# Kernel tuning notes

Measured on AMD Instinct MI355X. Metric: run time of the kernel, lower is better.

## Reference

```python
import jax, jax.numpy as jnp
import numpy as np

M, B, U, D = 65536, 128, 256, 512
USAGE_DECAY = 0.95

def _l2n(x, axis):
    # tf.nn.l2_normalize semantics (K.l2_normalize)
    return x / jnp.sqrt(jnp.maximum(jnp.sum(x * x, axis=axis, keepdims=True), 1e-12))

def _lstm_cell(x, h, c, kernel, rec_kernel, bias):
    # Keras LSTMCell: gates in order i, f, c, o
    z = x @ kernel + h @ rec_kernel + bias  # [B, 4U]
    zi, zf, zc, zo = jnp.split(z, 4, axis=-1)
    i = jax.nn.sigmoid(zi)
    f = jax.nn.sigmoid(zf)
    c_new = f * c + i * jnp.tanh(zc)
    o = jax.nn.sigmoid(zo)
    h_new = o * jnp.tanh(c_new)
    return h_new, c_new

def setup_inputs() -> dict:
    key = jax.random.key(0)
    ks = jax.random.split(key, 10)
    return {
        "inputs": jax.random.normal(ks[0], (B, D), jnp.float32),
        "r_tm1": jnp.zeros((B, U), jnp.float32),
        "m_tm1": jax.random.uniform(ks[1], (M, U), jnp.float32),
        "c_wu_tm1": jax.random.uniform(ks[2], (M, B), jnp.float32),
        "c_wlu_tm1": jnp.zeros((M, B), jnp.float32),
        "c_wr_tm1": jax.random.uniform(ks[3], (M, B), jnp.float32),
        "h_tm1": jax.random.normal(ks[4], (B, U), jnp.float32) * 0.1,
        "cc_tm1": jax.random.normal(ks[5], (B, U), jnp.float32) * 0.1,
        "kernel": jax.random.normal(ks[6], (D + U, 4 * U), jnp.float32) * 0.02,
        "rec_kernel": jax.random.normal(ks[7], (U, 4 * U), jnp.float32) * 0.02,
        "bias": jnp.zeros((4 * U,), jnp.float32),
        "write_gate": jax.random.normal(ks[8], (1,), jnp.float32),
    }

def reference(inputs, r_tm1, m_tm1, c_wu_tm1, c_wlu_tm1, c_wr_tm1,
              h_tm1, cc_tm1, kernel, rec_kernel, bias, write_gate):
    # Controller step on [inputs, r_tm1]
    ctrl_in = jnp.concatenate([inputs, r_tm1], axis=1)          # [B, D+U]
    key_list, cc = _lstm_cell(ctrl_in, h_tm1, cc_tm1, kernel, rec_kernel, bias)  # [B, U]

    wg = jax.nn.sigmoid(write_gate)                              # [1]
    # NOTE: faithful to source -- scalar (1 - wg) is ADDED elementwise, then c_wlu added
    c_ww = wg * c_wr_tm1 + (1.0 - wg) + c_wlu_tm1                # [M, B]

    # cosine-similarity addressing
    cos = _l2n(key_list, 1) @ _l2n(m_tm1, 1).T                   # [B, M]
    # K.softmax on the transposed matrix => softmax over the BATCH axis (faithful)
    c_wr = jax.nn.softmax(cos.T, axis=-1)                        # [M, B]
    read = c_wr.T @ m_tm1                                        # [B, U]

    c_wu = USAGE_DECAY * c_wu_tm1 + c_wr + c_ww                  # [M, B]

    # top_k(c_wu.T, M): v.T[-1,:] is the per-batch minimum over slots
    mins = jnp.min(c_wu, axis=0)                                 # [B]
    min_idx = jnp.argmin(c_wu, axis=0)                           # [B]
    b_star = jnp.argmin(mins)                                    # scalar
    i_star = min_idx[b_star]                                     # global least-used slot

    c_wlu = (c_wu <= mins[None, :]).astype(jnp.float32)          # [M, B]

    # zeroing_matrix = one_hot(i_star broadcast to B cols, on=0, off=1) [M,B];
    # dot(zeroing[M,B], ones[B,U]) -> rows = B except zeroed row (faithful B scaling)
    keep = 1.0 - jax.nn.one_hot(i_star, M, dtype=jnp.float32)    # [M]
    memory = (float(B) * keep)[:, None] * m_tm1                  # [M, U]
    memory = c_ww @ key_list + memory                            # [M, U]

    return (read, memory, c_wu, c_wlu, c_wr, key_list, cc)
```

## Files before the change

kernel.cpp:

```cpp
#include <hip/hip_runtime.h>
#include <math.h>

#define NM 65536
#define NB 128
#define NU 256
#define ND 512

constexpr size_t OUT_READ = 0;
constexpr size_t OUT_MEM  = 32768;
constexpr size_t OUT_CWU  = OUT_MEM + 16777216;
constexpr size_t OUT_CWLU = OUT_CWU + 8388608;
constexpr size_t OUT_CWR  = OUT_CWLU + 8388608;
constexpr size_t OUT_KEY  = OUT_CWR + 8388608;
constexpr size_t OUT_CC   = OUT_KEY + 32768;

constexpr size_t WS_KLNT   = 0;
constexpr size_t WS_MINENC = 131072;
constexpr size_t WS_MINS   = 132096;
constexpr size_t WS_ISTAR  = 132608;
constexpr size_t WS_PART   = 135168;

__device__ __forceinline__ unsigned fenc(float x) {
    unsigned u = __float_as_uint(x);
    return (u & 0x80000000u) ? ~u : (u | 0x80000000u);
}
__device__ __forceinline__ float fdec(unsigned e) {
    unsigned u = (e & 0x80000000u) ? (e ^ 0x80000000u) : ~e;
    return __uint_as_float(u);
}
__device__ __forceinline__ float sigm(float x) { return 1.0f / (1.0f + expf(-x)); }

__global__ __launch_bounds__(256) void k_lstm(
    const float* __restrict__ xin_g, const float* __restrict__ r_tm1,
    const float* __restrict__ h_tm1, const float* __restrict__ cc_tm1,
    const float* __restrict__ Wk, const float* __restrict__ Wr,
    const float* __restrict__ bias, float* __restrict__ out,
    float* __restrict__ klnT, unsigned long long* __restrict__ minenc)
{
    const int b = blockIdx.x, t = threadIdx.x;
    __shared__ float xin[ND + NU];
    __shared__ float hh[NU];
    __shared__ float red[NU];
    for (int k = t; k < ND; k += 256) xin[k] = xin_g[b * ND + k];
    xin[ND + t] = r_tm1[b * NU + t];
    hh[t] = h_tm1[b * NU + t];
    out[OUT_READ + b * NU + t] = 0.f;
    if (b == 0 && t < NB) minenc[t] = ~0ULL;
    __syncthreads();

    float zi = bias[t], zf = bias[NU + t], zc = bias[2 * NU + t], zo = bias[3 * NU + t];
    #pragma unroll 4
    for (int k = 0; k < ND + NU; ++k) {
        const float x = xin[k];
        const float* w = Wk + (size_t)k * (4 * NU);
        zi += x * w[t]; zf += x * w[NU + t]; zc += x * w[2 * NU + t]; zo += x * w[3 * NU + t];
    }
    #pragma unroll 4
    for (int k = 0; k < NU; ++k) {
        const float x = hh[k];
        const float* w = Wr + (size_t)k * (4 * NU);
        zi += x * w[t]; zf += x * w[NU + t]; zc += x * w[2 * NU + t]; zo += x * w[3 * NU + t];
    }
    const float gi = sigm(zi), gf = sigm(zf), gc = tanhf(zc), go = sigm(zo);
    const float cold = cc_tm1[b * NU + t];
    const float cn = __fadd_rn(__fmul_rn(gf, cold), __fmul_rn(gi, gc));
    const float hn = __fmul_rn(go, tanhf(cn));
    out[OUT_KEY + b * NU + t] = hn;
    out[OUT_CC + b * NU + t] = cn;
    red[t] = hn * hn;
    __syncthreads();
    for (int s = 128; s > 0; s >>= 1) { if (t < s) red[t] += red[t + s]; __syncthreads(); }
    const float nrm = sqrtf(fmaxf(red[0], 1e-12f));
    klnT[t * NB + b] = hn / nrm;
}

__global__ __launch_bounds__(256, 2) void k_dot(
    const float* __restrict__ mT, const float* __restrict__ klnT,
    const float* __restrict__ cwr_t, const float* __restrict__ cwlu_t,
    const float* __restrict__ cwu_t, const float* __restrict__ wgp,
    float* __restrict__ out, unsigned long long* __restrict__ minenc)
{
    __shared__ float ms[2][8][128];
    __shared__ float sp[32][132];
    __shared__ float rn_s[128];
    const int t = threadIdx.x, w = t >> 6, l = t & 63;
    const int tx = t & 15, ty = t >> 4;
    const int sb = blockIdx.x * 128;
    const int sl = t & 127, ug = t >> 7;

    #pragma unroll 4
    for (int i = 0; i < 32; ++i) {
        const int s = w * 32 + i;
        const float4 mv = *(const float4*)(mT + (size_t)(sb + s) * NU + l * 4);
        float ss = mv.x * mv.x + mv.y * mv.y + mv.z * mv.z + mv.w * mv.w;
        #pragma unroll
        for (int d = 1; d < 64; d <<= 1) ss += __shfl_xor(ss, d);
        if (l == 0) rn_s[s] = sqrtf(fmaxf(ss, 1e-12f));
    }

    float acc[8][8];
    #pragma unroll
    for (int i = 0; i < 8; ++i)
        #pragma unroll
        for (int j = 0; j < 8; ++j) acc[i][j] = 0.f;

    float4 kva[4], kvb[4];
    #pragma unroll
    for (int u = 0; u < 4; ++u) {
        kva[u] = *(const float4*)(klnT + (size_t)u * NB + tx * 4);
        kvb[u] = *(const float4*)(klnT + (size_t)u * NB + tx * 4 + 64);
    }
    float4 gm = *(const float4*)(mT + (size_t)(sb + sl) * NU + ug * 4);

    for (int c = 0; c < 32; ++c) {
        const int cb = c & 1;
        ms[cb][ug * 4 + 0][sl] = gm.x;
        ms[cb][ug * 4 + 1][sl] = gm.y;
        ms[cb][ug * 4 + 2][sl] = gm.z;
        ms[cb][ug * 4 + 3][sl] = gm.w;
        if (c < 31)
            gm = *(const float4*)(mT + (size_t)(sb + sl) * NU + (c + 1) * 8 + ug * 4);
        __syncthreads();
        #pragma unroll
        for (int u8 = 0; u8 < 8; ++u8) {
            const int r = u8 & 3;
            const float4 sv0 = *(const float4*)&ms[cb][u8][ty * 4];
            const float4 sv1 = *(const float4*)&ms[cb][u8][64 + ty * 4];
            const float svv[8] = {sv0.x, sv0.y, sv0.z, sv0.w, sv1.x, sv1.y, sv1.z, sv1.w};
            const float kvv[8] = {kva[r].x, kva[r].y, kva[r].z, kva[r].w,
                                  kvb[r].x, kvb[r].y, kvb[r].z, kvb[r].w};
            #pragma unroll
            for (int i = 0; i < 8; ++i)
                #pragma unroll
                for (int j = 0; j < 8; ++j)
                    acc[i][j] += svv[i] * kvv[j];
            const int un = (c * 8 + u8 + 4) & 255;
            kva[r] = *(const float4*)(klnT + (size_t)un * NB + tx * 4);
            kvb[r] = *(const float4*)(klnT + (size_t)un * NB + tx * 4 + 64);
        }
    }

    const float wg = sigm(wgp[0]);
    const float omw = __fsub_rn(1.f, wg);
    unsigned long long lmin0 = ~0ULL, lmin1 = ~0ULL;
    #pragma unroll
    for (int g = 0; g < 4; ++g) {
        if ((ty >> 3) == (g & 1)) {
            const int h = g >> 1;
            const int sl0 = (ty & 7) * 4;
            #pragma unroll
            for (int q = 0; q < 4; ++q) {
                *(float4*)&sp[sl0 + q][tx * 4] =
                    make_float4(acc[h * 4 + q][0], acc[h * 4 + q][1], acc[h * 4 + q][2], acc[h * 4 + q][3]);
                *(float4*)&sp[sl0 + q][64 + tx * 4] =
                    make_float4(acc[h * 4 + q][4], acc[h * 4 + q][5], acc[h * 4 + q][6], acc[h * 4 + q][7]);
            }
        }
        __syncthreads();
        #pragma unroll 2
        for (int i = 0; i < 8; ++i) {
            const int s = 32 * g + w * 8 + i;
            const int m = sb + s;
            const float2 dv = *(const float2*)&sp[s - 32 * g][2 * l];
            const float rnv = rn_s[s];
            const float2 wrt = ((const float2*)(cwr_t + (size_t)m * NB))[l];
            const float2 wlu = ((const float2*)(cwlu_t + (size_t)m * NB))[l];
            const float2 wut = ((const float2*)(cwu_t + (size_t)m * NB))[l];
            const float c0 = dv.x / rnv, c1 = dv.y / rnv;
            float mx = fmaxf(c0, c1);
            #pragma unroll
            for (int d = 1; d < 64; d <<= 1) mx = fmaxf(mx, __shfl_xor(mx, d));
            const float e0 = expf(c0 - mx), e1 = expf(c1 - mx);
            float sm = e0 + e1;
            #pragma unroll
            for (int d = 1; d < 64; d <<= 1) sm += __shfl_xor(sm, d);
            const float w0 = e0 / sm, w1 = e1 / sm;
            const float cww0 = __fadd_rn(__fadd_rn(__fmul_rn(wg, wrt.x), omw), wlu.x);
            const float cww1 = __fadd_rn(__fadd_rn(__fmul_rn(wg, wrt.y), omw), wlu.y);
            const float cu0 = __fadd_rn(__fadd_rn(__fmul_rn(0.95f, wut.x), w0), cww0);
            const float cu1 = __fadd_rn(__fadd_rn(__fmul_rn(0.95f, wut.y), w1), cww1);
            ((float2*)(out + OUT_CWR))[(size_t)m * 64 + l] = make_float2(w0, w1);
            ((float2*)(out + OUT_CWU))[(size_t)m * 64 + l] = make_float2(cu0, cu1);
            const unsigned long long e0u = (((unsigned long long)fenc(cu0)) << 32) | (unsigned)m;
            const unsigned long long e1u = (((unsigned long long)fenc(cu1)) << 32) | (unsigned)m;
            lmin0 = (e0u < lmin0) ? e0u : lmin0;
            lmin1 = (e1u < lmin1) ? e1u : lmin1;
        }
        __syncthreads();
    }
    atomicMin(&minenc[2 * l], lmin0);
    atomicMin(&minenc[2 * l + 1], lmin1);
}

__global__ void k_argmin(const unsigned long long* __restrict__ minenc,
                         float* __restrict__ mins, unsigned* __restrict__ istar)
{
    __shared__ unsigned long long red[NB];
    const int t = threadIdx.x;
    const unsigned long long e = minenc[t];
    const unsigned enc32 = (unsigned)(e >> 32);
    mins[t] = fdec(enc32);
    red[t] = (((unsigned long long)enc32) << 32) | (unsigned)t;
    __syncthreads();
    for (int s = 64; s > 0; s >>= 1) {
        if (t < s) { const unsigned long long o = red[t + s]; if (o < red[t]) red[t] = o; }
        __syncthreads();
    }
    if (t == 0) {
        const unsigned bstar = (unsigned)(red[0] & 0xFFFFFFFFu);
        istar[0] = (unsigned)(minenc[bstar] & 0xFFFFFFFFu);
    }
}

__global__ __launch_bounds__(256, 1) void k_mem(
    const float* __restrict__ mT,
    const float* __restrict__ cwr_t, const float* __restrict__ cwlu_t,
    const float* __restrict__ wgp, const float* __restrict__ mins,
    const unsigned* __restrict__ istar_p, float* __restrict__ out)
{
    __shared__ float key[NB][NU];
    __shared__ float cww[32][NB];
    __shared__ float minsb[NB];
    const int t = threadIdx.x, w = t >> 6, l = t & 63;
    const int u0 = l * 4;
    const int sl = t >> 3, sb = (t & 7) * 16;

    for (int i = t; i < NB * NU / 4; i += 256)
        ((float4*)key)[i] = ((const float4*)(out + OUT_KEY))[i];
    if (t < NB) minsb[t] = mins[t];

    const float wg = sigm(wgp[0]);
    const float omw = __fsub_rn(1.f, wg);
    const int istar = (int)istar_p[0];
    const int base = blockIdx.x * 256;

    float4 wr[4], lu[4], wu[4], pm[8];
    #pragma unroll
    for (int k = 0; k < 4; ++k) {
        const size_t row = (size_t)(base + sl) * NB + sb + 4 * k;
        wr[k] = *(const float4*)(cwr_t + row);
        lu[k] = *(const float4*)(cwlu_t + row);
        wu[k] = *(const float4*)(out + OUT_CWU + row);
    }
    #pragma unroll
    for (int j = 0; j < 8; ++j)
        pm[j] = *(const float4*)(mT + (size_t)(base + w * 8 + j) * NU + u0);
    __syncthreads();

    for (int p = 0; p < 8; ++p) {
        const int sp = base + p * 32;
        #pragma unroll
        for (int k = 0; k < 4; ++k) {
            float4 cw;
            cw.x = __fadd_rn(__fadd_rn(__fmul_rn(wg, wr[k].x), omw), lu[k].x);
            cw.y = __fadd_rn(__fadd_rn(__fmul_rn(wg, wr[k].y), omw), lu[k].y);
            cw.z = __fadd_rn(__fadd_rn(__fmul_rn(wg, wr[k].z), omw), lu[k].z);
            cw.w = __fadd_rn(__fadd_rn(__fmul_rn(wg, wr[k].w), omw), lu[k].w);
            *(float4*)&cww[sl][sb + 4 * k] = cw;
            const float4 mb = *(const float4*)&minsb[sb + 4 * k];
            float4 wl;
            wl.x = (wu[k].x <= mb.x) ? 1.f : 0.f;
            wl.y = (wu[k].y <= mb.y) ? 1.f : 0.f;
            wl.z = (wu[k].z <= mb.z) ? 1.f : 0.f;
            wl.w = (wu[k].w <= mb.w) ? 1.f : 0.f;
            *(float4*)(out + OUT_CWLU + (size_t)(sp + sl) * NB + sb + 4 * k) = wl;
        }
        __syncthreads();
        float4 pmn[8];
        if (p < 7) {
            #pragma unroll
            for (int k = 0; k < 4; ++k) {
                const size_t row = (size_t)(sp + 32 + sl) * NB + sb + 4 * k;
                wr[k] = *(const float4*)(cwr_t + row);
                lu[k] = *(const float4*)(cwlu_t + row);
                wu[k] = *(const float4*)(out + OUT_CWU + row);
            }
            #pragma unroll
            for (int j = 0; j < 8; ++j)
                pmn[j] = *(const float4*)(mT + (size_t)(sp + 32 + w * 8 + j) * NU + u0);
        }
        float4 acc[8];
        #pragma unroll
        for (int j = 0; j < 8; ++j) acc[j] = make_float4(0.f, 0.f, 0.f, 0.f);
        for (int b0 = 0; b0 < NB; b0 += 4) {
            const float4 kv0 = *(const float4*)&key[b0 + 0][u0];
            const float4 kv1 = *(const float4*)&key[b0 + 1][u0];
            const float4 kv2 = *(const float4*)&key[b0 + 2][u0];
            const float4 kv3 = *(const float4*)&key[b0 + 3][u0];
            #pragma unroll
            for (int j = 0; j < 8; ++j) {
                const float4 cw = *(const float4*)&cww[w * 8 + j][b0];
                acc[j].x += cw.x * kv0.x; acc[j].y += cw.x * kv0.y; acc[j].z += cw.x * kv0.z; acc[j].w += cw.x * kv0.w;
                acc[j].x += cw.y * kv1.x; acc[j].y += cw.y * kv1.y; acc[j].z += cw.y * kv1.z; acc[j].w += cw.y * kv1.w;
                acc[j].x += cw.z * kv2.x; acc[j].y += cw.z * kv2.y; acc[j].z += cw.z * kv2.z; acc[j].w += cw.z * kv2.w;
                acc[j].x += cw.w * kv3.x; acc[j].y += cw.w * kv3.y; acc[j].z += cw.w * kv3.z; acc[j].w += cw.w * kv3.w;
            }
        }
        #pragma unroll
        for (int j = 0; j < 8; ++j) {
            const int s = sp + w * 8 + j;
            const float kf = (s == istar) ? 0.f : 128.f;
            float4 o;
            o.x = acc[j].x + kf * pm[j].x;
            o.y = acc[j].y + kf * pm[j].y;
            o.z = acc[j].z + kf * pm[j].z;
            o.w = acc[j].w + kf * pm[j].w;
            *(float4*)(out + OUT_MEM + (size_t)s * NU + u0) = o;
            if (p < 7) pm[j] = pmn[j];
        }
        __syncthreads();
    }
}

template <int USE_PART>
__global__ __launch_bounds__(256) void k_read(
    const float* __restrict__ mT, float* __restrict__ out, float* __restrict__ part)
{
    __shared__ float m_ch[2][8][128];
    __shared__ float cwr_ch[2][8][128];
    const int t = threadIdx.x;
    const int r = blockIdx.x, ri = r >> 1, uh = r & 1;
    const int s0 = ri * 256;
    const int b0 = (t & 15) * 8, u0 = (t >> 4) * 8;
    const int ssl = t >> 5, sul = (t & 31) * 4;

    float4 acc[8][2];
    #pragma unroll
    for (int bi = 0; bi < 8; ++bi) { acc[bi][0] = make_float4(0,0,0,0); acc[bi][1] = make_float4(0,0,0,0); }

    float4 pm = *(const float4*)(mT + (size_t)(s0 + ssl) * NU + uh * 128 + sul);
    float4 pc = *(const float4*)(out + OUT_CWR + (size_t)(s0 + ssl) * NB + sul);

    for (int c = 0; c < 32; ++c) {
        const int buf = c & 1;
        *(float4*)&m_ch[buf][ssl][sul] = pm;
        *(float4*)&cwr_ch[buf][ssl][sul] = pc;
        __syncthreads();
        if (c + 1 < 32) {
            const size_t sn = (size_t)(s0 + (c + 1) * 8 + ssl);
            pm = *(const float4*)(mT + sn * NU + uh * 128 + sul);
            pc = *(const float4*)(out + OUT_CWR + sn * NB + sul);
        }
        #pragma unroll
        for (int sj = 0; sj < 8; ++sj) {
            const float4 ca = *(const float4*)&cwr_ch[buf][sj][b0];
            const float4 cb = *(const float4*)&cwr_ch[buf][sj][b0 + 4];
            const float4 ma = *(const float4*)&m_ch[buf][sj][u0];
            const float4 mb = *(const float4*)&m_ch[buf][sj][u0 + 4];
            const float cwa[8] = {ca.x, ca.y, ca.z, ca.w, cb.x, cb.y, cb.z, cb.w};
            #pragma unroll
            for (int bi = 0; bi < 8; ++bi) {
                acc[bi][0].x += cwa[bi] * ma.x; acc[bi][0].y += cwa[bi] * ma.y;
                acc[bi][0].z += cwa[bi] * ma.z; acc[bi][0].w += cwa[bi] * ma.w;
                acc[bi][1].x += cwa[bi] * mb.x; acc[bi][1].y += cwa[bi] * mb.y;
                acc[bi][1].z += cwa[bi] * mb.z; acc[bi][1].w += cwa[bi] * mb.w;
            }
        }
    }

    if (USE_PART) {
        float* dst = part + (size_t)r * (128 * 128);
        #pragma unroll
        for (int bi = 0; bi < 8; ++bi) {
            *(float4*)(dst + (size_t)(b0 + bi) * 128 + u0) = acc[bi][0];
            *(float4*)(dst + (size_t)(b0 + bi) * 128 + u0 + 4) = acc[bi][1];
        }
    } else {
        #pragma unroll
        for (int bi = 0; bi < 8; ++bi) {
            const float v[8] = {acc[bi][0].x, acc[bi][0].y, acc[bi][0].z, acc[bi][0].w,
                                acc[bi][1].x, acc[bi][1].y, acc[bi][1].z, acc[bi][1].w};
            #pragma unroll
            for (int q = 0; q < 8; ++q)
                atomicAdd(out + OUT_READ + (size_t)(b0 + bi) * NU + uh * 128 + u0 + q, v[q]);
        }
    }
}

__global__ __launch_bounds__(256) void k_redread(const float* __restrict__ part,
                                                 float* __restrict__ out)
{
    const int b = blockIdx.x, u = threadIdx.x;
    const int uh = u >> 7, ul = u & 127;
    float s = 0.f;
    #pragma unroll 4
    for (int ri = 0; ri < 256; ++ri)
        s += part[((size_t)(ri * 2 + uh) * 128 + b) * 128 + ul];
    out[OUT_READ + b * NU + u] = s;
}

extern "C" void kernel_launch(void* const* d_in, const int* in_sizes, int n_in,
                              void* d_out, int out_size, void* d_ws, size_t ws_size,
                              hipStream_t stream)
{
    const float* inputs    = (const float*)d_in[0];
    const float* r_tm1     = (const float*)d_in[1];
    const float* m_tm1     = (const float*)d_in[2];
    const float* c_wu_tm1  = (const float*)d_in[3];
    const float* c_wlu_tm1 = (const float*)d_in[4];
    const float* c_wr_tm1  = (const float*)d_in[5];
    const float* h_tm1     = (const float*)d_in[6];
    const float* cc_tm1    = (const float*)d_in[7];
    const float* Wk        = (const float*)d_in[8];
    const float* Wr        = (const float*)d_in[9];
    const float* bias      = (const float*)d_in[10];
    const float* wgate     = (const float*)d_in[11];
    float* out = (float*)d_out;
    char* ws = (char*)d_ws;

    float* klnT = (float*)(ws + WS_KLNT);
    unsigned long long* minenc = (unsigned long long*)(ws + WS_MINENC);
    float* mins = (float*)(ws + WS_MINS);
    unsigned* istar = (unsigned*)(ws + WS_ISTAR);
    float* part = (float*)(ws + WS_PART);
    const bool use_part = ws_size >= WS_PART + (size_t)512 * 128 * 128 * 4;

    hipLaunchKernelGGL(k_lstm, dim3(128), dim3(256), 0, stream,
                       inputs, r_tm1, h_tm1, cc_tm1, Wk, Wr, bias, out, klnT, minenc);
    hipLaunchKernelGGL(k_dot, dim3(512), dim3(256), 0, stream,
                       m_tm1, klnT, c_wr_tm1, c_wlu_tm1, c_wu_tm1, wgate, out, minenc);
    hipLaunchKernelGGL(k_argmin, dim3(1), dim3(128), 0, stream, minenc, mins, istar);
    hipLaunchKernelGGL(k_mem, dim3(256), dim3(256), 0, stream,
                       m_tm1, c_wr_tm1, c_wlu_tm1, wgate, mins, istar, out);
    if (use_part) {
        hipLaunchKernelGGL((k_read<1>), dim3(512), dim3(256), 0, stream, m_tm1, out, part);
        hipLaunchKernelGGL(k_redread, dim3(128), dim3(256), 0, stream, part, out);
    } else {
        hipLaunchKernelGGL((k_read<0>), dim3(512), dim3(256), 0, stream, m_tm1, out, part);
    }
}
```

Measured before the change: 472.6 us.

## Restructure cosine GEMM so each wavefront owns its slots, removing block barriers

The similarity GEMM in k_dot is reorganized so that each 64-lane wavefront computes its own 32 memory slots against all 128 batch columns. Memory rows are kept in registers, and key vectors are staged per wavefront in LDS. Block-wide __syncthreads in the main loop and the epilogue are removed, and the epilogue scratch becomes per-wavefront. This is meant to cut barrier stalls and improve overlap, at the cost of more LDS traffic for the key operand and redundant per-wave key staging. There is also a risk of missing intra-wave ordering between LDS writes and reads without a barrier.

```diff
diff --git a/kernel.cpp b/kernel.cpp
--- a/kernel.cpp
+++ b/kernel.cpp
@@ -80,13 +80,22 @@
     const float* __restrict__ cwu_t, const float* __restrict__ wgp,
     float* __restrict__ out, unsigned long long* __restrict__ minenc)
 {
-    __shared__ float ms[2][8][128];
-    __shared__ float sp[32][132];
+    __shared__ float kvs[4][8][128];
+    __shared__ float sp[4][8][132];
     __shared__ float rn_s[128];
     const int t = threadIdx.x, w = t >> 6, l = t & 63;
-    const int tx = t & 15, ty = t >> 4;
+    const int sg = l >> 3, bg = l & 7;
     const int sb = blockIdx.x * 128;
-    const int sl = t & 127, ug = t >> 7;
+    const float* mrow = mT + (size_t)(sb + w * 32 + sg * 4) * NU;
+
+    float4 gk[4];
+    #pragma unroll
+    for (int q = 0; q < 4; ++q)
+        gk[q] = *(const float4*)(klnT + q * 256 + l * 4);
+    float4 mm[4], mn[4];
+    #pragma unroll
+    for (int i = 0; i < 4; ++i)
+        mm[i] = *(const float4*)(mrow + (size_t)i * NU);
 
     #pragma unroll 4
     for (int i = 0; i < 32; ++i) {
@@ -98,45 +107,49 @@
         if (l == 0) rn_s[s] = sqrtf(fmaxf(ss, 1e-12f));
     }
 
-    float acc[8][8];
-    #pragma unroll
-    for (int i = 0; i < 8; ++i)
-        #pragma unroll
-        for (int j = 0; j < 8; ++j) acc[i][j] = 0.f;
-
-    float4 kva[4], kvb[4];
-    #pragma unroll
-    for (int u = 0; u < 4; ++u) {
-        kva[u] = *(const float4*)(klnT + (size_t)u * NB + tx * 4);
-        kvb[u] = *(const float4*)(klnT + (size_t)u * NB + tx * 4 + 64);
-    }
-    float4 gm = *(const float4*)(mT + (size_t)(sb + sl) * NU + ug * 4);
+    float acc[4][16];
+    #pragma unroll
+    for (int i = 0; i < 4; ++i)
+        #pragma unroll
+        for (int j = 0; j < 16; ++j) acc[i][j] = 0.f;
 
     for (int c = 0; c < 32; ++c) {
-        const int cb = c & 1;
-        ms[cb][ug * 4 + 0][sl] = gm.x;
-        ms[cb][ug * 4 + 1][sl] = gm.y;
-        ms[cb][ug * 4 + 2][sl] = gm.z;
-        ms[cb][ug * 4 + 3][sl] = gm.w;
-        if (c < 31)
-            gm = *(const float4*)(mT + (size_t)(sb + sl) * NU + (c + 1) * 8 + ug * 4);
-        __syncthreads();
-        #pragma unroll
-        for (int u8 = 0; u8 < 8; ++u8) {
-            const int r = u8 & 3;
-            const float4 sv0 = *(const float4*)&ms[cb][u8][ty * 4];
-            const float4 sv1 = *(const float4*)&ms[cb][u8][64 + ty * 4];
-            const float svv[8] = {sv0.x, sv0.y, sv0.z, sv0.w, sv1.x, sv1.y, sv1.z, sv1.w};
-            const float kvv[8] = {kva[r].x, kva[r].y, kva[r].z, kva[r].w,
-                                  kvb[r].x, kvb[r].y, kvb[r].z, kvb[r].w};
-            #pragma unroll
-            for (int i = 0; i < 8; ++i)
+        #pragma unroll
+        for (int q = 0; q < 4; ++q)
+            *(float4*)&kvs[w][0][l * 4 + q * 256] = gk[q];
+        const int cn = (c < 31) ? c + 1 : 0;
+        #pragma unroll
+        for (int q = 0; q < 4; ++q)
+            gk[q] = *(const float4*)(klnT + (size_t)cn * 1024 + q * 256 + l * 4);
+        #pragma unroll
+        for (int h = 0; h < 2; ++h) {
+            const int cm = (h == 0) ? c : cn;
+            const int hn = 1 - h;
+            #pragma unroll
+            for (int i = 0; i < 4; ++i)
+                mn[i] = *(const float4*)(mrow + (size_t)i * NU + cm * 8 + hn * 4);
+            #pragma unroll
+            for (int u4 = 0; u4 < 4; ++u4) {
+                const int u8 = h * 4 + u4;
+                float4 kvv[4];
                 #pragma unroll
-                for (int j = 0; j < 8; ++j)
-                    acc[i][j] += svv[i] * kvv[j];
-            const int un = (c * 8 + u8 + 4) & 255;
-            kva[r] = *(const float4*)(klnT + (size_t)un * NB + tx * 4);
-            kvb[r] = *(const float4*)(klnT + (size_t)un * NB + tx * 4 + 64);
+                for (int k = 0; k < 4; ++k)
+                    kvv[k] = *(const float4*)&kvs[w][u8][bg * 4 + k * 32];
+                #pragma unroll
+                for (int i = 0; i < 4; ++i) {
+                    const float sv = (u4 == 0) ? mm[i].x : (u4 == 1) ? mm[i].y
+                                   : (u4 == 2) ? mm[i].z : mm[i].w;
+                    #pragma unroll
+                    for (int k = 0; k < 4; ++k) {
+                        acc[i][k * 4 + 0] += sv * kvv[k].x;
+                        acc[i][k * 4 + 1] += sv * kvv[k].y;
+                        acc[i][k * 4 + 2] += sv * kvv[k].z;
+                        acc[i][k * 4 + 3] += sv * kvv[k].w;
+                    }
+                }
+            }
+            #pragma unroll
+            for (int i = 0; i < 4; ++i) mm[i] = mn[i];
         }
     }
 
@@ -145,23 +158,21 @@
     unsigned long long lmin0 = ~0ULL, lmin1 = ~0ULL;
     #pragma unroll
     for (int g = 0; g < 4; ++g) {
-        if ((ty >> 3) == (g & 1)) {
-            const int h = g >> 1;
-            const int sl0 = (ty & 7) * 4;
-            #pragma unroll
-            for (int q = 0; q < 4; ++q) {
-                *(float4*)&sp[sl0 + q][tx * 4] =
-                    make_float4(acc[h * 4 + q][0], acc[h * 4 + q][1], acc[h * 4 + q][2], acc[h * 4 + q][3]);
-                *(float4*)&sp[sl0 + q][64 + tx * 4] =
-                    make_float4(acc[h * 4 + q][4], acc[h * 4 + q][5], acc[h * 4 + q][6], acc[h * 4 + q][7]);
-            }
-        }
-        __syncthreads();
+        if ((sg >> 1) == g) {
+            const int d = sg & 1;
+            #pragma unroll
+            for (int i = 0; i < 4; ++i)
+                #pragma unroll
+                for (int k = 0; k < 4; ++k)
+                    *(float4*)&sp[w][d * 4 + i][bg * 4 + k * 32] =
+                        make_float4(acc[i][k * 4 + 0], acc[i][k * 4 + 1],
+                                    acc[i][k * 4 + 2], acc[i][k * 4 + 3]);
+        }
         #pragma unroll 2
         for (int i = 0; i < 8; ++i) {
-            const int s = 32 * g + w * 8 + i;
+            const int s = w * 32 + g * 8 + i;
             const int m = sb + s;
-            const float2 dv = *(const float2*)&sp[s - 32 * g][2 * l];
+            const float2 dv = *(const float2*)&sp[w][i][2 * l];
             const float rnv = rn_s[s];
             const float2 wrt = ((const float2*)(cwr_t + (size_t)m * NB))[l];
             const float2 wlu = ((const float2*)(cwlu_t + (size_t)m * NB))[l];
@@ -186,7 +197,6 @@
             lmin0 = (e0u < lmin0) ? e0u : lmin0;
             lmin1 = (e1u < lmin1) ? e1u : lmin1;
         }
-        __syncthreads();
     }
     atomicMin(&minenc[2 * l], lmin0);
     atomicMin(&minenc[2 * l + 1], lmin1);
```

Result: slower. 506.8 us (+7.2%).
